# Performance work log

Measured on AMD Instinct MI355X. Metric: run time of the kernel, lower is better.

Reference implementation:

```python
import jax, jax.numpy as jnp
import numpy as np

B, T, C = 8, 2048, 1024
HEAD = 64
BLOCK = 2048  # block_size == max_size == ramp_size


def setup_inputs() -> dict:
    key = jax.random.key(0)
    kx, kq, kk, kv = jax.random.split(key, 4)
    x = jax.random.normal(kx, (B, T, C), dtype=jnp.float32)
    # torch Linear(n_embd, head_size, bias=False): store as (C, HEAD) for x @ W
    s = 1.0 / np.sqrt(C)
    Wq = jax.random.uniform(kq, (C, HEAD), dtype=jnp.float32, minval=-s, maxval=s)
    Wk = jax.random.uniform(kk, (C, HEAD), dtype=jnp.float32, minval=-s, maxval=s)
    Wv = jax.random.uniform(kv, (C, HEAD), dtype=jnp.float32, minval=-s, maxval=s)
    # adaptive_span current_val parameter, shape (1,1,1), init 0
    current_val = jnp.zeros((1, 1, 1), dtype=jnp.float32)
    return {"x": x, "Wq": Wq, "Wk": Wk, "Wv": Wv, "current_val": current_val}


def reference(x, Wq, Wk, Wv, current_val):
    Bb, Tt, Cc = x.shape
    q = x @ Wq  # (B,T,H)
    k = x @ Wk
    v = x @ Wv
    scale = 1.0 / jnp.sqrt(jnp.asarray(HEAD, dtype=x.dtype))
    scores = jnp.einsum('bth,bsh->bts', q, k) * scale  # (B,T,T)
    causal = jnp.tril(jnp.ones((Tt, Tt), dtype=bool))
    scores = jnp.where(causal, scores, -jnp.inf)
    w = jax.nn.softmax(scores, axis=-1)
    # adaptive span post-softmax mask (T == max_size here, so no slicing)
    template = jnp.linspace(1.0 - BLOCK, 0.0, BLOCK, dtype=x.dtype)  # (T,)
    span = template + current_val * BLOCK  # (1,1,T)
    span = jnp.clip(span / BLOCK + 1.0, 0.0, 1.0)
    w = w * span
    w = w / (w.sum(-1, keepdims=True) + 1e-8)
    # dropout p=0 (eval) -> identity
    out = jnp.einsum('bts,bsh->bth', w, v)  # (B,T,H)
    return out
```

## Files before the change

kernel.cpp:

```cpp
#include <hip/hip_runtime.h>
#include <hip/hip_bf16.h>

#define BSZ 8
#define T 2048
#define C 1024
#define H 64
#define M (BSZ*T)

typedef __attribute__((ext_vector_type(4))) float f32x4;
typedef __attribute__((ext_vector_type(8))) short bf16x8;
typedef __attribute__((ext_vector_type(4))) short s16x4;
typedef __attribute__((ext_vector_type(8))) short s16x8;

static __device__ __forceinline__ short f2bf(float f) {
  union { float f; unsigned u; } c; c.f = f;
  unsigned u = c.u;
  u = (u + 0x7fffu + ((u >> 16) & 1u)) >> 16;
  return (short)u;
}

__global__ __launch_bounds__(256) void k_wt(const float* __restrict__ Wq,
                                            const float* __restrict__ Wk,
                                            const float* __restrict__ Wv,
                                            short* __restrict__ wt) {
  int idx = blockIdx.x * 256 + threadIdx.x;
  int c = idx & (C - 1);
  int n = idx >> 10;
  int w = n >> 6;
  int h = n & (H - 1);
  const float* W = (w == 0) ? Wq : (w == 1) ? Wk : Wv;
  wt[idx] = f2bf(W[c * H + h]);
}

__global__ __launch_bounds__(256) void k_qkv(const float* __restrict__ x,
                                             const short* __restrict__ wt,
                                             short* __restrict__ qb,
                                             short* __restrict__ kb,
                                             short* __restrict__ vt) {
  __shared__ short xs[2][32 * 64];
  __shared__ short wl[2][192 * 64];
  const int tid = threadIdx.x;
  const int m0 = blockIdx.x * 32;
  const int lane = tid & 63;
  const int wid = tid >> 6;
  const int g16 = lane >> 4, l16 = lane & 15;
  const int row0 = (wid & 1) * 16;
  const int nc0 = (wid >> 1) * 96;

  f32x4 acc[6];
  #pragma unroll
  for (int i = 0; i < 6; ++i) acc[i] = (f32x4){0.f, 0.f, 0.f, 0.f};

  const int xr = tid >> 4;
  const int xc4 = (tid & 15) * 4;
  const int xsw = xc4 ^ ((xr & 7) << 3);
  const int wr = tid >> 3;
  const int wc8 = (tid & 7) * 8;
  const int wsw = wc8 ^ ((wr & 7) << 3);
  const int fsw = (l16 & 7) << 3;

  float4 xA0, xA1, xB0, xB1;
  s16x8 wA0, wA1, wA2, wA3, wA4, wA5;
  s16x8 wB0, wB1, wB2, wB3, wB4, wB5;

#define QKV_LOAD(S, kc) do { \
    x##S##0 = *(const float4*)&x[(size_t)(m0 + xr) * C + (kc) + xc4]; \
    x##S##1 = *(const float4*)&x[(size_t)(m0 + xr + 16) * C + (kc) + xc4]; \
    w##S##0 = *(const s16x8*)&wt[(wr +   0) * C + (kc) + wc8]; \
    w##S##1 = *(const s16x8*)&wt[(wr +  32) * C + (kc) + wc8]; \
    w##S##2 = *(const s16x8*)&wt[(wr +  64) * C + (kc) + wc8]; \
    w##S##3 = *(const s16x8*)&wt[(wr +  96) * C + (kc) + wc8]; \
    w##S##4 = *(const s16x8*)&wt[(wr + 128) * C + (kc) + wc8]; \
    w##S##5 = *(const s16x8*)&wt[(wr + 160) * C + (kc) + wc8]; \
  } while (0)

#define QKV_STORE(S, buf) do { \
    s16x4 h0 = { f2bf((x##S##0).x), f2bf((x##S##0).y), f2bf((x##S##0).z), f2bf((x##S##0).w) }; \
    s16x4 h1 = { f2bf((x##S##1).x), f2bf((x##S##1).y), f2bf((x##S##1).z), f2bf((x##S##1).w) }; \
    *(s16x4*)&xs[buf][xr * 64 + xsw] = h0; \
    *(s16x4*)&xs[buf][(xr + 16) * 64 + xsw] = h1; \
    *(s16x8*)&wl[buf][(wr +   0) * 64 + wsw] = w##S##0; \
    *(s16x8*)&wl[buf][(wr +  32) * 64 + wsw] = w##S##1; \
    *(s16x8*)&wl[buf][(wr +  64) * 64 + wsw] = w##S##2; \
    *(s16x8*)&wl[buf][(wr +  96) * 64 + wsw] = w##S##3; \
    *(s16x8*)&wl[buf][(wr + 128) * 64 + wsw] = w##S##4; \
    *(s16x8*)&wl[buf][(wr + 160) * 64 + wsw] = w##S##5; \
  } while (0)

#define QKV_COMPUTE(buf) do { \
    _Pragma("unroll") \
    for (int ks = 0; ks < 2; ++ks) { \
      bf16x8 a = *(const bf16x8*)&xs[buf][(row0 + l16) * 64 + ((ks * 32 + g16 * 8) ^ fsw)]; \
      _Pragma("unroll") \
      for (int nt = 0; nt < 6; ++nt) { \
        bf16x8 bfr = *(const bf16x8*)&wl[buf][(nc0 + nt * 16 + l16) * 64 + ((ks * 32 + g16 * 8) ^ fsw)]; \
        acc[nt] = __builtin_amdgcn_mfma_f32_16x16x32_bf16(a, bfr, acc[nt], 0, 0, 0); \
      } \
    } \
  } while (0)

  QKV_LOAD(A, 0);
  QKV_STORE(A, 0);
  QKV_LOAD(B, 64);
  __syncthreads();

  #pragma unroll 1
  for (int ii = 0; ii < 8; ++ii) {
    if (ii < 7) QKV_LOAD(A, (2 * ii + 2) * 64);
    QKV_STORE(B, 1);
    QKV_COMPUTE(0);
    __syncthreads();
    if (ii < 7) {
      QKV_LOAD(B, (2 * ii + 3) * 64);
      QKV_STORE(A, 0);
    }
    QKV_COMPUTE(1);
    if (ii < 7) __syncthreads();
  }
#undef QKV_LOAD
#undef QKV_STORE
#undef QKV_COMPUTE

  const int r0 = row0 + g16 * 4;
  #pragma unroll
  for (int nt = 0; nt < 6; ++nt) {
    const int nglob = nc0 + nt * 16;
    const int which = nglob >> 6;
    const int col = (nglob & 63) + l16;
    #pragma unroll
    for (int j = 0; j < 4; ++j) {
      const int tg = m0 + r0 + j;
      const short val = f2bf(acc[nt][j]);
      if (which == 0)      qb[tg * H + col] = val;
      else if (which == 1) kb[tg * H + col] = val;
      else {
        const int b = tg >> 11, tl = tg & (T - 1);
        vt[((b << 6) + col) * T + tl] = val;
      }
    }
  }
}

__global__ __launch_bounds__(512, 2) void k_attn(const short* __restrict__ qb,
                                                 const short* __restrict__ kb,
                                                 const short* __restrict__ vt,
                                                 const float* __restrict__ cvp,
                                                 float* __restrict__ out) {
  __shared__ float Ow[8][16][68];
  __shared__ float mw[8][16];
  __shared__ float Lw[8][16];
  const int pid = blockIdx.x;
  const int b = pid & 7;
  const int pr = pid >> 3;
  const int q0A = pr << 4, q0B = (127 - pr) << 4;
  const int nitA = (q0A + 47) >> 5;
  const int nitB = (q0B + 47) >> 5;
  const int NT = nitA + nitB;
  int wA = (8 * nitA + (NT >> 1)) / NT;
  wA = wA < 1 ? 1 : (wA > 7 ? 7 : wA);

  const int tid = threadIdx.x;
  const int wid = tid >> 6;
  const int lane = tid & 63;
  const int g16 = lane >> 4, l16 = lane & 15;
  const float cv = cvp[0];
  const float SCL = 0.125f * 1.44269504f;

  const bool onA = (wid < wA);
  const int q0 = onA ? q0A : q0B;
  const int nitW = onA ? nitA : nitB;
  const int nwt = onA ? wA : 8 - wA;
  const int wg = onA ? wid : wid - wA;
  const int npw = (nitW + nwt - 1) / nwt;
  const int lo = wg * npw;
  const int hi = (lo + npw < nitW) ? lo + npw : nitW;

  const short* qp = qb + ((size_t)(b << 11) + q0 + l16) * H + g16 * 8;
  bf16x8 qf0 = *(const bf16x8*)qp;
  bf16x8 qf1 = *(const bf16x8*)(qp + 32);
  const int qg = q0 + l16;

  const int gsel = (g16 & 1) << 5;
  const int addrA = (gsel + l16) << 2;
  const int addrB = (gsel + 16 + l16) << 2;
  const bool ghi = (g16 >= 2);

  float m = -3e38f, L = 0.f;
  f32x4 O[4];
  #pragma unroll
  for (int t4 = 0; t4 < 4; ++t4) O[t4] = (f32x4){0.f, 0.f, 0.f, 0.f};

  if (lo < hi) {
    const short* kp = kb + ((size_t)(b << 11) + lo * 32 + l16) * H + g16 * 8;
    const short* vp = vt + ((size_t)(b << 6) + l16) * T + lo * 32 + g16 * 8;
    bf16x8 kA0 = *(const bf16x8*)kp;
    bf16x8 kA1 = *(const bf16x8*)(kp + 32);
    bf16x8 kA2 = *(const bf16x8*)(kp + 16 * H);
    bf16x8 kA3 = *(const bf16x8*)(kp + 16 * H + 32);
    kp += 32 * H;
    bf16x8 kB0 = kA0, kB1 = kA1, kB2 = kA2, kB3 = kA3;
    if (lo + 1 < hi) {
      kB0 = *(const bf16x8*)kp;
      kB1 = *(const bf16x8*)(kp + 32);
      kB2 = *(const bf16x8*)(kp + 16 * H);
      kB3 = *(const bf16x8*)(kp + 16 * H + 32);
      kp += 32 * H;
    }
    f32x4 s0c = {0.f,0.f,0.f,0.f}, s1c = {0.f,0.f,0.f,0.f};
    s0c = __builtin_amdgcn_mfma_f32_16x16x32_bf16(kA0, qf0, s0c, 0, 0, 0);
    s0c = __builtin_amdgcn_mfma_f32_16x16x32_bf16(kA1, qf1, s0c, 0, 0, 0);
    s1c = __builtin_amdgcn_mfma_f32_16x16x32_bf16(kA2, qf0, s1c, 0, 0, 0);
    s1c = __builtin_amdgcn_mfma_f32_16x16x32_bf16(kA3, qf1, s1c, 0, 0, 0);

    auto astep = [&](int it,
                     bf16x8 kn0, bf16x8 kn1, bf16x8 kn2, bf16x8 kn3,
                     bf16x8& kl0, bf16x8& kl1, bf16x8& kl2, bf16x8& kl3) {
      bf16x8 v0 = *(const bf16x8*)vp;
      bf16x8 v1 = *(const bf16x8*)(vp + 16 * T);
      bf16x8 v2 = *(const bf16x8*)(vp + 32 * T);
      bf16x8 v3 = *(const bf16x8*)(vp + 48 * T);
      if (it + 2 < hi) {
        kl0 = *(const bf16x8*)kp;
        kl1 = *(const bf16x8*)(kp + 32);
        kl2 = *(const bf16x8*)(kp + 16 * H);
        kl3 = *(const bf16x8*)(kp + 16 * H + 32);
        kp += 32 * H;
      }
      f32x4 n0 = {0.f,0.f,0.f,0.f}, n1 = {0.f,0.f,0.f,0.f};
      if (it + 1 < hi) {
        n0 = __builtin_amdgcn_mfma_f32_16x16x32_bf16(kn0, qf0, n0, 0, 0, 0);
        n0 = __builtin_amdgcn_mfma_f32_16x16x32_bf16(kn1, qf1, n0, 0, 0, 0);
        n1 = __builtin_amdgcn_mfma_f32_16x16x32_bf16(kn2, qf0, n1, 0, 0, 0);
        n1 = __builtin_amdgcn_mfma_f32_16x16x32_bf16(kn3, qf1, n1, 0, 0, 0);
      }

      const int kv0 = it << 5;
      const int kvb = kv0 + g16 * 4;
      const bool diag = (kv0 + 31 > q0);
      float sv[8];
      if (diag) {
        #pragma unroll
        for (int r = 0; r < 8; ++r) {
          const int kvg = kvb + ((r >> 2) << 4) + (r & 3);
          const float s = ((r < 4) ? s0c[r] : s1c[r - 4]) * SCL;
          sv[r] = (kvg <= qg) ? s : -1e30f;
        }
      } else {
        #pragma unroll
        for (int r = 0; r < 8; ++r)
          sv[r] = ((r < 4) ? s0c[r] : s1c[r - 4]) * SCL;
      }
      float pmax = fmaxf(fmaxf(fmaxf(sv[0], sv[1]), fmaxf(sv[2], sv[3])),
                         fmaxf(fmaxf(sv[4], sv[5]), fmaxf(sv[6], sv[7])));
      if (!__all(pmax <= m + 7.f)) {
        float v = pmax;
        v = fmaxf(v, __shfl_xor(v, 16, 64));
        v = fmaxf(v, __shfl_xor(v, 32, 64));
        const float mn = fmaxf(m, v);
        const float al = exp2f(m - mn);
        m = mn;
        L *= al;
        #pragma unroll
        for (int t4 = 0; t4 < 4; ++t4) O[t4] *= al;
      }
      float p[8];
      #pragma unroll
      for (int r = 0; r < 8; ++r) {
        const int kvg = kvb + ((r >> 2) << 4) + (r & 3);
        const float sp = fminf(fmaxf((float)(kvg + 1) * (1.f / 2048.f) + cv, 0.f), 1.f);
        p[r] = exp2f(sv[r] - m) * sp;
      }
      if (diag) {
        #pragma unroll
        for (int r = 0; r < 8; ++r) {
          const int kvg = kvb + ((r >> 2) << 4) + (r & 3);
          p[r] = (kvg <= qg) ? p[r] : 0.f;
        }
      }
      L += ((p[0] + p[1]) + (p[2] + p[3])) + ((p[4] + p[5]) + (p[6] + p[7]));

      union { float f; unsigned u; } a0, a1;
      unsigned d0, d1, d2, d3;
      a0.f = p[0]; a1.f = p[1]; d0 = (a0.u >> 16) | (a1.u & 0xffff0000u);
      a0.f = p[2]; a1.f = p[3]; d1 = (a0.u >> 16) | (a1.u & 0xffff0000u);
      a0.f = p[4]; a1.f = p[5]; d2 = (a0.u >> 16) | (a1.u & 0xffff0000u);
      a0.f = p[6]; a1.f = p[7]; d3 = (a0.u >> 16) | (a1.u & 0xffff0000u);
      const int lo0 = __builtin_amdgcn_ds_bpermute(addrA, (int)d0);
      const int lo1 = __builtin_amdgcn_ds_bpermute(addrA, (int)d1);
      const int lo2 = __builtin_amdgcn_ds_bpermute(addrB, (int)d0);
      const int lo3 = __builtin_amdgcn_ds_bpermute(addrB, (int)d1);
      const int hi0 = __builtin_amdgcn_ds_bpermute(addrA, (int)d2);
      const int hi1 = __builtin_amdgcn_ds_bpermute(addrA, (int)d3);
      const int hi2 = __builtin_amdgcn_ds_bpermute(addrB, (int)d2);
      const int hi3 = __builtin_amdgcn_ds_bpermute(addrB, (int)d3);
      union { int w[4]; bf16x8 v8; } pu;
      pu.w[0] = ghi ? hi0 : lo0;
      pu.w[1] = ghi ? hi1 : lo1;
      pu.w[2] = ghi ? hi2 : lo2;
      pu.w[3] = ghi ? hi3 : lo3;
      const bf16x8 pa = pu.v8;

      O[0] = __builtin_amdgcn_mfma_f32_16x16x32_bf16(v0, pa, O[0], 0, 0, 0);
      O[1] = __builtin_amdgcn_mfma_f32_16x16x32_bf16(v1, pa, O[1], 0, 0, 0);
      O[2] = __builtin_amdgcn_mfma_f32_16x16x32_bf16(v2, pa, O[2], 0, 0, 0);
      O[3] = __builtin_amdgcn_mfma_f32_16x16x32_bf16(v3, pa, O[3], 0, 0, 0);

      s0c = n0; s1c = n1;
      vp += 32;
    };

    #pragma unroll 1
    for (int itb = lo; itb < hi; itb += 2) {
      astep(itb, kB0, kB1, kB2, kB3, kA0, kA1, kA2, kA3);
      if (itb + 1 < hi)
        astep(itb + 1, kA0, kA1, kA2, kA3, kB0, kB1, kB2, kB3);
    }
  }

  float Lr = L;
  Lr += __shfl_xor(Lr, 16, 64);
  Lr += __shfl_xor(Lr, 32, 64);
  if (g16 == 0) { mw[wid][l16] = m; Lw[wid][l16] = Lr; }
  #pragma unroll
  for (int t4 = 0; t4 < 4; ++t4)
    *(f32x4*)&Ow[wid][l16][t4 * 16 + g16 * 4] = O[t4];
  __syncthreads();

  {
    const int r32 = tid >> 4;
    const int c4 = (tid & 15) << 2;
    const bool rowA = (r32 < 16);
    const int r = rowA ? r32 : r32 - 16;
    const int w0 = rowA ? 0 : wA;
    const int w1 = rowA ? wA : 8;
    const int q0r = rowA ? q0A : q0B;
    float Mx = -3e38f;
    for (int w = w0; w < w1; ++w) Mx = fmaxf(Mx, mw[w][r]);
    float Ls = 0.f;
    f32x4 o = (f32x4){0.f, 0.f, 0.f, 0.f};
    for (int w = w0; w < w1; ++w) {
      const float fw = exp2f(mw[w][r] - Mx);
      Ls += Lw[w][r] * fw;
      f32x4 ow = *(const f32x4*)&Ow[w][r][c4];
      o += ow * fw;
    }
    o *= 1.f / (Ls + 1e-30f);
    *(f32x4*)&out[(size_t)((b << 11) + q0r + r) * H + c4] = o;
  }
}

extern "C" void kernel_launch(void* const* d_in, const int* in_sizes, int n_in,
                              void* d_out, int out_size, void* d_ws, size_t ws_size,
                              hipStream_t stream) {
  const float* x  = (const float*)d_in[0];
  const float* Wq = (const float*)d_in[1];
  const float* Wk = (const float*)d_in[2];
  const float* Wv = (const float*)d_in[3];
  const float* cv = (const float*)d_in[4];
  float* out = (float*)d_out;

  char* ws = (char*)d_ws;
  short* qb = (short*)(ws);
  short* kb = (short*)(ws + (size_t)M * H * 2);
  short* vt = (short*)(ws + (size_t)2 * M * H * 2);
  short* wt = (short*)(ws + (size_t)3 * M * H * 2);

  hipLaunchKernelGGL(k_wt, dim3(3 * H * C / 256), dim3(256), 0, stream, Wq, Wk, Wv, wt);
  hipLaunchKernelGGL(k_qkv, dim3(M / 32), dim3(256), 0, stream, x, wt, qb, kb, vt);
  hipLaunchKernelGGL(k_attn, dim3(BSZ * T / 32), dim3(512), 0, stream, qb, kb, vt, cv, out);
}
```

Before: 64.96 us.

## Load QKV weights via global_load_lds and feed x fragments directly from registers

The weight-transpose kernel now writes the bf16 weights pre-tiled into 64-column chunks with the LDS XOR swizzle already applied. The QKV projection kernel can then copy each chunk straight into shared memory with global_load_lds. Each lane also loads its own x row fragment from global memory and converts it to bf16 in registers, so the x shared-memory tile and its stores go away. This aims to cut LDS write traffic and VGPR staging, but it relies on the DMA writes being complete at the barrier and gives up coalescing on the x loads.

```diff
diff --git a/kernel.cpp b/kernel.cpp
--- a/kernel.cpp
+++ b/kernel.cpp
@@ -24,20 +24,23 @@
                                             const float* __restrict__ Wv,
                                             short* __restrict__ wt) {
   int idx = blockIdx.x * 256 + threadIdx.x;
-  int c = idx & (C - 1);
-  int n = idx >> 10;
-  int w = n >> 6;
-  int h = n & (H - 1);
+  const int chunk = idx / 12288;
+  const int rem = idx - chunk * 12288;
+  const int n = rem >> 6;
+  const int cs = rem & 63;
+  const int cin = cs ^ ((n & 7) << 3);
+  const int c = (chunk << 6) + cin;
+  const int w = n >> 6;
+  const int h = n & (H - 1);
   const float* W = (w == 0) ? Wq : (w == 1) ? Wk : Wv;
   wt[idx] = f2bf(W[c * H + h]);
 }
 
 __global__ __launch_bounds__(256) void k_qkv(const float* __restrict__ x,
-                                             const short* __restrict__ wt,
+                                             const short* __restrict__ wts,
                                              short* __restrict__ qb,
                                              short* __restrict__ kb,
                                              short* __restrict__ vt) {
-  __shared__ short xs[2][32 * 64];
   __shared__ short wl[2][192 * 64];
   const int tid = threadIdx.x;
   const int m0 = blockIdx.x * 32;
@@ -46,80 +49,71 @@
   const int g16 = lane >> 4, l16 = lane & 15;
   const int row0 = (wid & 1) * 16;
   const int nc0 = (wid >> 1) * 96;
+  const int fsw = (l16 & 7) << 3;
 
   f32x4 acc[6];
   #pragma unroll
   for (int i = 0; i < 6; ++i) acc[i] = (f32x4){0.f, 0.f, 0.f, 0.f};
 
-  const int xr = tid >> 4;
-  const int xc4 = (tid & 15) * 4;
-  const int xsw = xc4 ^ ((xr & 7) << 3);
-  const int wr = tid >> 3;
-  const int wc8 = (tid & 7) * 8;
-  const int wsw = wc8 ^ ((wr & 7) << 3);
-  const int fsw = (l16 & 7) << 3;
-
-  float4 xA0, xA1, xB0, xB1;
-  s16x8 wA0, wA1, wA2, wA3, wA4, wA5;
-  s16x8 wB0, wB1, wB2, wB3, wB4, wB5;
-
-#define QKV_LOAD(S, kc) do { \
-    x##S##0 = *(const float4*)&x[(size_t)(m0 + xr) * C + (kc) + xc4]; \
-    x##S##1 = *(const float4*)&x[(size_t)(m0 + xr + 16) * C + (kc) + xc4]; \
-    w##S##0 = *(const s16x8*)&wt[(wr +   0) * C + (kc) + wc8]; \
-    w##S##1 = *(const s16x8*)&wt[(wr +  32) * C + (kc) + wc8]; \
-    w##S##2 = *(const s16x8*)&wt[(wr +  64) * C + (kc) + wc8]; \
-    w##S##3 = *(const s16x8*)&wt[(wr +  96) * C + (kc) + wc8]; \
-    w##S##4 = *(const s16x8*)&wt[(wr + 128) * C + (kc) + wc8]; \
-    w##S##5 = *(const s16x8*)&wt[(wr + 160) * C + (kc) + wc8]; \
-  } while (0)
-
-#define QKV_STORE(S, buf) do { \
-    s16x4 h0 = { f2bf((x##S##0).x), f2bf((x##S##0).y), f2bf((x##S##0).z), f2bf((x##S##0).w) }; \
-    s16x4 h1 = { f2bf((x##S##1).x), f2bf((x##S##1).y), f2bf((x##S##1).z), f2bf((x##S##1).w) }; \
-    *(s16x4*)&xs[buf][xr * 64 + xsw] = h0; \
-    *(s16x4*)&xs[buf][(xr + 16) * 64 + xsw] = h1; \
-    *(s16x8*)&wl[buf][(wr +   0) * 64 + wsw] = w##S##0; \
-    *(s16x8*)&wl[buf][(wr +  32) * 64 + wsw] = w##S##1; \
-    *(s16x8*)&wl[buf][(wr +  64) * 64 + wsw] = w##S##2; \
-    *(s16x8*)&wl[buf][(wr +  96) * 64 + wsw] = w##S##3; \
-    *(s16x8*)&wl[buf][(wr + 128) * 64 + wsw] = w##S##4; \
-    *(s16x8*)&wl[buf][(wr + 160) * 64 + wsw] = w##S##5; \
-  } while (0)
-
-#define QKV_COMPUTE(buf) do { \
+  float4 xA0, xA1, xA2, xA3, xB0, xB1, xB2, xB3;
+
+#define DMA(ii, buf) do { \
+    const short* gsrc = wts + (size_t)(ii) * 12288 + wid * 512 + lane * 8; \
+    short* ldsb = &wl[buf][wid * 512]; \
     _Pragma("unroll") \
-    for (int ks = 0; ks < 2; ++ks) { \
-      bf16x8 a = *(const bf16x8*)&xs[buf][(row0 + l16) * 64 + ((ks * 32 + g16 * 8) ^ fsw)]; \
-      _Pragma("unroll") \
-      for (int nt = 0; nt < 6; ++nt) { \
-        bf16x8 bfr = *(const bf16x8*)&wl[buf][(nc0 + nt * 16 + l16) * 64 + ((ks * 32 + g16 * 8) ^ fsw)]; \
-        acc[nt] = __builtin_amdgcn_mfma_f32_16x16x32_bf16(a, bfr, acc[nt], 0, 0, 0); \
-      } \
+    for (int j = 0; j < 6; ++j) { \
+      __builtin_amdgcn_global_load_lds( \
+          (const __attribute__((address_space(1))) void*)(gsrc + j * 2048), \
+          (__attribute__((address_space(3))) void*)(ldsb + j * 2048), \
+          16, 0, 0); \
     } \
   } while (0)
 
-  QKV_LOAD(A, 0);
-  QKV_STORE(A, 0);
-  QKV_LOAD(B, 64);
+#define XLOAD(S, kc) do { \
+    const float* xb = &x[(size_t)(m0 + row0 + l16) * C + (kc) + g16 * 8]; \
+    x##S##0 = *(const float4*)(xb); \
+    x##S##1 = *(const float4*)(xb + 4); \
+    x##S##2 = *(const float4*)(xb + 32); \
+    x##S##3 = *(const float4*)(xb + 36); \
+  } while (0)
+
+#define COMPUTE(buf, S) do { \
+    bf16x8 a0 = { f2bf((x##S##0).x), f2bf((x##S##0).y), f2bf((x##S##0).z), f2bf((x##S##0).w), \
+                  f2bf((x##S##1).x), f2bf((x##S##1).y), f2bf((x##S##1).z), f2bf((x##S##1).w) }; \
+    bf16x8 a1 = { f2bf((x##S##2).x), f2bf((x##S##2).y), f2bf((x##S##2).z), f2bf((x##S##2).w), \
+                  f2bf((x##S##3).x), f2bf((x##S##3).y), f2bf((x##S##3).z), f2bf((x##S##3).w) }; \
+    _Pragma("unroll") \
+    for (int nt = 0; nt < 6; ++nt) { \
+      bf16x8 b0 = *(const bf16x8*)&wl[buf][(nc0 + nt * 16 + l16) * 64 + ((g16 * 8) ^ fsw)]; \
+      acc[nt] = __builtin_amdgcn_mfma_f32_16x16x32_bf16(a0, b0, acc[nt], 0, 0, 0); \
+    } \
+    _Pragma("unroll") \
+    for (int nt = 0; nt < 6; ++nt) { \
+      bf16x8 b1 = *(const bf16x8*)&wl[buf][(nc0 + nt * 16 + l16) * 64 + ((32 + g16 * 8) ^ fsw)]; \
+      acc[nt] = __builtin_amdgcn_mfma_f32_16x16x32_bf16(a1, b1, acc[nt], 0, 0, 0); \
+    } \
+  } while (0)
+
+  XLOAD(A, 0);
+  DMA(0, 0);
   __syncthreads();
 
   #pragma unroll 1
   for (int ii = 0; ii < 8; ++ii) {
-    if (ii < 7) QKV_LOAD(A, (2 * ii + 2) * 64);
-    QKV_STORE(B, 1);
-    QKV_COMPUTE(0);
+    DMA(2 * ii + 1, 1);
+    XLOAD(B, (2 * ii + 1) * 64);
+    COMPUTE(0, A);
     __syncthreads();
     if (ii < 7) {
-      QKV_LOAD(B, (2 * ii + 3) * 64);
-      QKV_STORE(A, 0);
-    }
-    QKV_COMPUTE(1);
+      DMA(2 * ii + 2, 0);
+      XLOAD(A, (2 * ii + 2) * 64);
+    }
+    COMPUTE(1, B);
     if (ii < 7) __syncthreads();
   }
-#undef QKV_LOAD
-#undef QKV_STORE
-#undef QKV_COMPUTE
+#undef DMA
+#undef XLOAD
+#undef COMPUTE
 
   const int r0 = row0 + g16 * 4;
   #pragma unroll
```

New measurement: 72.27 us. +11.2%, slower.
